# Kernel tuning notes

Measured on AMD Instinct MI355X. Metric: run time of the kernel, lower is better.

The kernel has to match this reference:

```python
import jax, jax.numpy as jnp
import numpy as np

N_NODES = 50000
N_EDGES = 600000
HIDDEN = 128


def setup_inputs() -> dict:
    key = jax.random.key(0)
    ks = jax.random.split(key, 8)
    x = jax.random.normal(ks[0], (N_NODES, HIDDEN), dtype=jnp.float32)
    edge_index = jax.random.randint(ks[1], (2, N_EDGES), 0, N_NODES, dtype=jnp.int32)
    s = 1.0 / np.sqrt(HIDDEN)
    # PyG SAGEConv: lin_l applied to aggregated neighbors (with bias), lin_r to root (no bias)
    W1l = jax.random.uniform(ks[2], (HIDDEN, HIDDEN), jnp.float32, -s, s)
    b1l = jax.random.uniform(ks[3], (HIDDEN,), jnp.float32, -s, s)
    W1r = jax.random.uniform(ks[4], (HIDDEN, HIDDEN), jnp.float32, -s, s)
    W2l = jax.random.uniform(ks[5], (HIDDEN, HIDDEN), jnp.float32, -s, s)
    b2l = jax.random.uniform(ks[6], (HIDDEN,), jnp.float32, -s, s)
    W2r = jax.random.uniform(ks[7], (HIDDEN, HIDDEN), jnp.float32, -s, s)
    return {"x": x, "edge_index": edge_index, "W1l": W1l, "b1l": b1l,
            "W1r": W1r, "W2l": W2l, "b2l": b2l, "W2r": W2r}


def _sage_conv(x, src, dst, Wl, bl, Wr):
    # mean aggregation of source features at destination nodes
    msg_sum = jax.ops.segment_sum(x[src], dst, num_segments=N_NODES)  # [N, H]
    deg = jax.ops.segment_sum(jnp.ones((src.shape[0],), x.dtype), dst,
                              num_segments=N_NODES)  # [N]
    agg = msg_sum / jnp.maximum(deg, 1.0)[:, None]
    return agg @ Wl.T + bl + x @ Wr.T


def reference(x, edge_index, W1l, b1l, W1r, W2l, b2l, W2r):
    src, dst = edge_index[0], edge_index[1]
    h = jax.nn.relu(_sage_conv(x, src, dst, W1l, b1l, W1r))
    out = _sage_conv(h, src, dst, W2l, b2l, W2r)
    return out
```

## Files before the change

kernel.cpp:

```cpp
#include <hip/hip_runtime.h>
#include <hip/hip_bf16.h>

#define N_NODES 50000
#define N_EDGES 600000
#define HID 128
#define SCAN_BLOCKS ((N_NODES + 255) / 256)

typedef __attribute__((ext_vector_type(8))) __bf16 bf16x8;
typedef __attribute__((ext_vector_type(4))) float f32x4;

static __device__ __forceinline__ unsigned short f2b(float v) {
    return __builtin_bit_cast(unsigned short, (__bf16)v);
}


#define NCAST (N_NODES * HID / 8)
#define NVT   (2 * 128 * 256 / 8)
#define NFILL (N_NODES / 4)
#define NPREP (NCAST + NVT + NFILL)

__global__ __launch_bounds__(256) void k_prep(const float* __restrict__ x,
                                              const float* __restrict__ W1l, const float* __restrict__ W1r,
                                              const float* __restrict__ W2l, const float* __restrict__ W2r,
                                              unsigned short* __restrict__ xb,
                                              unsigned short* __restrict__ V1,
                                              unsigned short* __restrict__ V2,
                                              int* __restrict__ fill) {
    int idx = blockIdx.x * 256 + threadIdx.x;
    if (idx < NCAST) {
        const float4* xp = (const float4*)(x + (size_t)idx * 8);
        float4 a = xp[0], b = xp[1];
        uint4 o;
        o.x = f2b(a.x) | ((unsigned)f2b(a.y) << 16);
        o.y = f2b(a.z) | ((unsigned)f2b(a.w) << 16);
        o.z = f2b(b.x) | ((unsigned)f2b(b.y) << 16);
        o.w = f2b(b.z) | ((unsigned)f2b(b.w) << 16);
        *(uint4*)(xb + (size_t)idx * 8) = o;
    } else if (idx < NCAST + NVT) {
        int t = idx - NCAST;
        int i0 = t * 8;
        int which = i0 >> 15;
        const float* Wl = which ? W2l : W1l;
        const float* Wr = which ? W2r : W1r;
        unsigned short* V = which ? V2 : V1;
        int ii = i0 & 32767;
        int j = ii >> 8, k0 = ii & 255;
        const float* Wp = (k0 < HID) ? (Wl + j * HID + k0) : (Wr + j * HID + (k0 - HID));
        const float4* wp4 = (const float4*)Wp;
        float4 a = wp4[0], b = wp4[1];
        uint4 o;
        o.x = f2b(a.x) | ((unsigned)f2b(a.y) << 16);
        o.y = f2b(a.z) | ((unsigned)f2b(a.w) << 16);
        o.z = f2b(b.x) | ((unsigned)f2b(b.y) << 16);
        o.w = f2b(b.z) | ((unsigned)f2b(b.w) << 16);
        *(uint4*)(V + ii) = o;
    } else if (idx < NPREP) {
        int z = idx - (NCAST + NVT);
        *(int4*)(fill + z * 4) = make_int4(0, 0, 0, 0);
    }
}


__global__ void k_deg(const int* __restrict__ dst, int* __restrict__ fill, int ne) {
    int e = blockIdx.x * blockDim.x + threadIdx.x;
    if (e < ne) atomicAdd(&fill[dst[e]], 1);
}

__global__ __launch_bounds__(256) void k_bsum(const int* __restrict__ fill, int* __restrict__ bsum, int n) {
    __shared__ int s[256];
    int tid = threadIdx.x;
    int i = blockIdx.x * 256 + tid;
    s[tid] = (i < n) ? fill[i] : 0;
    __syncthreads();
#pragma unroll
    for (int off = 128; off > 0; off >>= 1) {
        if (tid < off) s[tid] += s[tid + off];
        __syncthreads();
    }
    if (tid == 0) bsum[blockIdx.x] = s[0];
}

__global__ __launch_bounds__(256) void k_scan_bsum(int* __restrict__ bsum, int* __restrict__ row_off,
                                                   int nb, int n) {
    __shared__ int s[256];
    int tid = threadIdx.x;
    int v = (tid < nb) ? bsum[tid] : 0;
    s[tid] = v;
    __syncthreads();
#pragma unroll
    for (int off = 1; off < 256; off <<= 1) {
        int t = (tid >= off) ? s[tid - off] : 0;
        __syncthreads();
        s[tid] += t;
        __syncthreads();
    }
    if (tid < nb) bsum[tid] = s[tid] - v;
    if (tid == 255) row_off[n] = s[255];
}

__global__ __launch_bounds__(256) void k_write_off(int* __restrict__ fill, const int* __restrict__ bsum,
                                                   int* __restrict__ row_off, float* __restrict__ inv_deg,
                                                   int n) {
    __shared__ int s[256];
    int tid = threadIdx.x;
    int i = blockIdx.x * 256 + tid;
    int c = (i < n) ? fill[i] : 0;
    s[tid] = c;
    __syncthreads();
#pragma unroll
    for (int off = 1; off < 256; off <<= 1) {
        int t = (tid >= off) ? s[tid - off] : 0;
        __syncthreads();
        s[tid] += t;
        __syncthreads();
    }
    if (i < n) {
        row_off[i] = bsum[blockIdx.x] + s[tid] - c;
        inv_deg[i] = 1.0f / (float)max(c, 1);
        fill[i] = 0;
    }
}

__global__ void k_place(const int* __restrict__ src, const int* __restrict__ dst,
                        const int* __restrict__ row_off, int* __restrict__ fill,
                        int* __restrict__ csr, int ne) {
    int e = blockIdx.x * blockDim.x + threadIdx.x;
    if (e < ne) {
        int d = dst[e];
        int pos = atomicAdd(&fill[d], 1);
        csr[row_off[d] + pos] = src[e];
    }
}


static __device__ __forceinline__ void acc_bf2(uint2 v, float& a0, float& a1, float& a2, float& a3) {
    a0 += __uint_as_float(v.x << 16);
    a1 += __uint_as_float(v.x & 0xffff0000u);
    a2 += __uint_as_float(v.y << 16);
    a3 += __uint_as_float(v.y & 0xffff0000u);
}

__global__ __launch_bounds__(256) void k_agg(const unsigned short* __restrict__ xb,
                                             const int* __restrict__ csr,
                                             const int* __restrict__ row_off,
                                             const float* __restrict__ inv_deg,
                                             unsigned short* __restrict__ aggB, int n) {
    int g = (blockIdx.x * blockDim.x + threadIdx.x) >> 5;
    int lane = threadIdx.x & 31;
    if (g >= n) return;
    int e0 = row_off[g], e1 = row_off[g + 1];
    float a0 = 0.f, a1 = 0.f, a2 = 0.f, a3 = 0.f;
    int e = e0;
    for (; e + 4 <= e1; e += 4) {
        int s0 = csr[e + 0];
        int s1 = csr[e + 1];
        int s2 = csr[e + 2];
        int s3 = csr[e + 3];
        uint2 v0 = *(const uint2*)(xb + (size_t)s0 * HID + lane * 4);
        uint2 v1 = *(const uint2*)(xb + (size_t)s1 * HID + lane * 4);
        uint2 v2 = *(const uint2*)(xb + (size_t)s2 * HID + lane * 4);
        uint2 v3 = *(const uint2*)(xb + (size_t)s3 * HID + lane * 4);
        acc_bf2(v0, a0, a1, a2, a3);
        acc_bf2(v1, a0, a1, a2, a3);
        acc_bf2(v2, a0, a1, a2, a3);
        acc_bf2(v3, a0, a1, a2, a3);
    }
    if (e + 2 <= e1) {
        int s0 = csr[e + 0];
        int s1 = csr[e + 1];
        uint2 v0 = *(const uint2*)(xb + (size_t)s0 * HID + lane * 4);
        uint2 v1 = *(const uint2*)(xb + (size_t)s1 * HID + lane * 4);
        acc_bf2(v0, a0, a1, a2, a3);
        acc_bf2(v1, a0, a1, a2, a3);
        e += 2;
    }
    if (e < e1) {
        int s0 = csr[e];
        uint2 v0 = *(const uint2*)(xb + (size_t)s0 * HID + lane * 4);
        acc_bf2(v0, a0, a1, a2, a3);
    }
    float inv = inv_deg[g];
    ushort4 o;
    o.x = f2b(a0 * inv); o.y = f2b(a1 * inv); o.z = f2b(a2 * inv); o.w = f2b(a3 * inv);
    *(ushort4*)(aggB + (size_t)g * HID + lane * 4) = o;
}


__global__ __launch_bounds__(512) void k_gemm(const unsigned short* __restrict__ aggB,
                                              const unsigned short* __restrict__ xinB,
                                              const unsigned short* __restrict__ VT,
                                              const float* __restrict__ bias,
                                              float* __restrict__ outF,
                                              unsigned short* __restrict__ outB,
                                              int mode ,
                                              int nrows) {
    __shared__ char As[32768];
    __shared__ char Bs[32768];
    int tid = threadIdx.x;
    int w = tid >> 6, l = tid & 63;
    int r0 = blockIdx.x * 128;

    f32x4 acc[8] = {};

    int arow = w * 16 + (l & 15);
    int kgrp = (l >> 4) * 8;

    for (int p = 0; p < 2; ++p) {
        const unsigned short* Asrc = p ? xinB : aggB;
#pragma unroll
        for (int q = 0; q < 4; ++q) {
            int c = tid + q * 512;
            int m = c >> 4, c16 = c & 15;
            int gr = r0 + m;
            uint4 v = make_uint4(0, 0, 0, 0);
            if (gr < nrows) v = *(const uint4*)(Asrc + (size_t)gr * HID + c16 * 8);
            int byt = (m * 256 + c16 * 16) ^ ((m & 7) << 4);
            *(uint4*)(As + byt) = v;
        }
#pragma unroll
        for (int q = 0; q < 4; ++q) {
            int c = tid + q * 512;
            int j = c >> 4, c16 = c & 15;
            uint4 v = *(const uint4*)(VT + (size_t)j * 256 + p * 128 + c16 * 8);
            int byt = (j * 256 + c16 * 16) ^ ((j & 7) << 4);
            *(uint4*)(Bs + byt) = v;
        }
        __syncthreads();

#pragma unroll
        for (int s = 0; s < 4; ++s) {
            int koff = (s * 32 + kgrp) * 2;
            bf16x8 a = *(const bf16x8*)(As + ((arow * 256 + koff) ^ ((arow & 7) << 4)));
#pragma unroll
            for (int cc = 0; cc < 8; ++cc) {
                int brow = cc * 16 + (l & 15);
                bf16x8 b = *(const bf16x8*)(Bs + ((brow * 256 + koff) ^ ((brow & 7) << 4)));
                acc[cc] = __builtin_amdgcn_mfma_f32_16x16x32_bf16(a, b, acc[cc], 0, 0, 0);
            }
        }
        __syncthreads();
    }

    int lo = l & 15, hi = l >> 4;
#pragma unroll
    for (int cc = 0; cc < 8; ++cc) {
        int col = cc * 16 + lo;
        float bv = bias[col];
#pragma unroll
        for (int i = 0; i < 4; ++i) {
            int gr = r0 + w * 16 + hi * 4 + i;
            if (gr < nrows) {
                float v = acc[cc][i] + bv;
                if (mode) {
                    v = fmaxf(v, 0.f);
                    outB[(size_t)gr * HID + col] = f2b(v);
                } else {
                    outF[(size_t)gr * HID + col] = v;
                }
            }
        }
    }
}


extern "C" void kernel_launch(void* const* d_in, const int* in_sizes, int n_in,
                              void* d_out, int out_size, void* d_ws, size_t ws_size,
                              hipStream_t stream) {
    const float* x   = (const float*)d_in[0];
    const int*   ei  = (const int*)d_in[1];
    const float* W1l = (const float*)d_in[2];
    const float* b1l = (const float*)d_in[3];
    const float* W1r = (const float*)d_in[4];
    const float* W2l = (const float*)d_in[5];
    const float* b2l = (const float*)d_in[6];
    const float* W2r = (const float*)d_in[7];
    float* out = (float*)d_out;

    const int* src = ei;
    const int* dst = ei + N_EDGES;

    char* w = (char*)d_ws;
    unsigned short* aggB = (unsigned short*)(w);
    unsigned short* buf0 = (unsigned short*)(w + 12800000);
    int*   csr     = (int*)(w + 25600000);
    int*   row_off = (int*)(w + 28000000);
    int*   fill    = (int*)(w + 28200192);
    float* inv_deg = (float*)(w + 28400384);
    unsigned short* V1 = (unsigned short*)(w + 28600576);
    unsigned short* V2 = (unsigned short*)(w + 28666112);
    int*   bsum    = (int*)(w + 28731648);

    k_prep<<<(NPREP + 255) / 256, 256, 0, stream>>>(x, W1l, W1r, W2l, W2r, buf0, V1, V2, fill);

    k_deg<<<(N_EDGES + 255) / 256, 256, 0, stream>>>(dst, fill, N_EDGES);

    k_bsum<<<SCAN_BLOCKS, 256, 0, stream>>>(fill, bsum, N_NODES);
    k_scan_bsum<<<1, 256, 0, stream>>>(bsum, row_off, SCAN_BLOCKS, N_NODES);
    k_write_off<<<SCAN_BLOCKS, 256, 0, stream>>>(fill, bsum, row_off, inv_deg, N_NODES);

    k_place<<<(N_EDGES + 255) / 256, 256, 0, stream>>>(src, dst, row_off, fill, csr, N_EDGES);

    const int gemm_grid = (N_NODES + 127) / 128;

    k_agg<<<(N_NODES * 32 + 255) / 256, 256, 0, stream>>>(buf0, csr, row_off, inv_deg, aggB, N_NODES);
    k_gemm<<<gemm_grid, 512, 0, stream>>>(aggB, buf0, V1, b1l, out, buf0, 1, N_NODES);

    k_agg<<<(N_NODES * 32 + 255) / 256, 256, 0, stream>>>(buf0, csr, row_off, inv_deg, aggB, N_NODES);
    k_gemm<<<gemm_grid, 512, 0, stream>>>(aggB, buf0, V2, b2l, out, buf0, 0, N_NODES);
}
```

Before: 157.3 us.

## Merge offset scan into one atomic-cursor kernel, widen gather unroll, prefetch GEMM second half

The three-kernel scan (block sums, scan of sums, write offsets) is replaced by one kernel. Each block reserves its base offset through an atomicAdd on a global cursor, and per-node degree is stored so row ends come from start plus degree. Aggregation now unrolls the gather by 8 with a predicated tail, and the GEMM issues the global loads for the root-feature half into registers before the MFMA loop on the aggregated half runs. These changes cut launch count and expose more memory-level parallelism, at the cost of a non-monotonic CSR block order and higher register pressure.

```diff
diff --git a/kernel.cpp b/kernel.cpp
--- a/kernel.cpp
+++ b/kernel.cpp
@@ -25,7 +25,8 @@
                                               unsigned short* __restrict__ xb,
                                               unsigned short* __restrict__ V1,
                                               unsigned short* __restrict__ V2,
-                                              int* __restrict__ fill) {
+                                              int* __restrict__ fill,
+                                              int* __restrict__ cursor) {
     int idx = blockIdx.x * 256 + threadIdx.x;
     if (idx < NCAST) {
         const float4* xp = (const float4*)(x + (size_t)idx * 8);
@@ -57,6 +58,8 @@
     } else if (idx < NPREP) {
         int z = idx - (NCAST + NVT);
         *(int4*)(fill + z * 4) = make_int4(0, 0, 0, 0);
+    } else if (idx == NPREP) {
+        *cursor = 0;
     }
 }
 
@@ -66,26 +69,17 @@
     if (e < ne) atomicAdd(&fill[dst[e]], 1);
 }
 
-__global__ __launch_bounds__(256) void k_bsum(const int* __restrict__ fill, int* __restrict__ bsum, int n) {
+__global__ __launch_bounds__(256) void k_offsets(int* __restrict__ fill,
+                                                 int* __restrict__ row_start,
+                                                 int* __restrict__ dg,
+                                                 float* __restrict__ inv_deg,
+                                                 int* __restrict__ cursor, int n) {
     __shared__ int s[256];
+    __shared__ int base;
     int tid = threadIdx.x;
     int i = blockIdx.x * 256 + tid;
-    s[tid] = (i < n) ? fill[i] : 0;
-    __syncthreads();
-#pragma unroll
-    for (int off = 128; off > 0; off >>= 1) {
-        if (tid < off) s[tid] += s[tid + off];
-        __syncthreads();
-    }
-    if (tid == 0) bsum[blockIdx.x] = s[0];
-}
-
-__global__ __launch_bounds__(256) void k_scan_bsum(int* __restrict__ bsum, int* __restrict__ row_off,
-                                                   int nb, int n) {
-    __shared__ int s[256];
-    int tid = threadIdx.x;
-    int v = (tid < nb) ? bsum[tid] : 0;
-    s[tid] = v;
+    int c = (i < n) ? fill[i] : 0;
+    s[tid] = c;
     __syncthreads();
 #pragma unroll
     for (int off = 1; off < 256; off <<= 1) {
@@ -94,41 +88,24 @@
         s[tid] += t;
         __syncthreads();
     }
-    if (tid < nb) bsum[tid] = s[tid] - v;
-    if (tid == 255) row_off[n] = s[255];
-}
-
-__global__ __launch_bounds__(256) void k_write_off(int* __restrict__ fill, const int* __restrict__ bsum,
-                                                   int* __restrict__ row_off, float* __restrict__ inv_deg,
-                                                   int n) {
-    __shared__ int s[256];
-    int tid = threadIdx.x;
-    int i = blockIdx.x * 256 + tid;
-    int c = (i < n) ? fill[i] : 0;
-    s[tid] = c;
-    __syncthreads();
-#pragma unroll
-    for (int off = 1; off < 256; off <<= 1) {
-        int t = (tid >= off) ? s[tid - off] : 0;
-        __syncthreads();
-        s[tid] += t;
-        __syncthreads();
-    }
+    if (tid == 255) base = atomicAdd(cursor, s[255]);
+    __syncthreads();
     if (i < n) {
-        row_off[i] = bsum[blockIdx.x] + s[tid] - c;
+        row_start[i] = base + s[tid] - c;
+        dg[i] = c;
         inv_deg[i] = 1.0f / (float)max(c, 1);
         fill[i] = 0;
     }
 }
 
 __global__ void k_place(const int* __restrict__ src, const int* __restrict__ dst,
-                        const int* __restrict__ row_off, int* __restrict__ fill,
+                        const int* __restrict__ row_start, int* __restrict__ fill,
                         int* __restrict__ csr, int ne) {
     int e = blockIdx.x * blockDim.x + threadIdx.x;
     if (e < ne) {
         int d = dst[e];
         int pos = atomicAdd(&fill[d], 1);
-        csr[row_off[d] + pos] = src[e];
+        csr[row_start[d] + pos] = src[e];
     }
 }
 
@@ -142,42 +119,41 @@
 
 __global__ __launch_bounds__(256) void k_agg(const unsigned short* __restrict__ xb,
                                              const int* __restrict__ csr,
-                                             const int* __restrict__ row_off,
+                                             const int* __restrict__ row_start,
+                                             const int* __restrict__ dg,
                                              const float* __restrict__ inv_deg,
                                              unsigned short* __restrict__ aggB, int n) {
     int g = (blockIdx.x * blockDim.x + threadIdx.x) >> 5;
     int lane = threadIdx.x & 31;
     if (g >= n) return;
-    int e0 = row_off[g], e1 = row_off[g + 1];
+    int e0 = row_start[g];
+    int e1 = e0 + dg[g];
     float a0 = 0.f, a1 = 0.f, a2 = 0.f, a3 = 0.f;
     int e = e0;
-    for (; e + 4 <= e1; e += 4) {
-        int s0 = csr[e + 0];
-        int s1 = csr[e + 1];
-        int s2 = csr[e + 2];
-        int s3 = csr[e + 3];
+    for (; e + 8 <= e1; e += 8) {
+        int s0 = csr[e + 0], s1 = csr[e + 1], s2 = csr[e + 2], s3 = csr[e + 3];
+        int s4 = csr[e + 4], s5 = csr[e + 5], s6 = csr[e + 6], s7 = csr[e + 7];
         uint2 v0 = *(const uint2*)(xb + (size_t)s0 * HID + lane * 4);
         uint2 v1 = *(const uint2*)(xb + (size_t)s1 * HID + lane * 4);
         uint2 v2 = *(const uint2*)(xb + (size_t)s2 * HID + lane * 4);
         uint2 v3 = *(const uint2*)(xb + (size_t)s3 * HID + lane * 4);
-        acc_bf2(v0, a0, a1, a2, a3);
-        acc_bf2(v1, a0, a1, a2, a3);
-        acc_bf2(v2, a0, a1, a2, a3);
-        acc_bf2(v3, a0, a1, a2, a3);
-    }
-    if (e + 2 <= e1) {
-        int s0 = csr[e + 0];
-        int s1 = csr[e + 1];
-        uint2 v0 = *(const uint2*)(xb + (size_t)s0 * HID + lane * 4);
-        uint2 v1 = *(const uint2*)(xb + (size_t)s1 * HID + lane * 4);
-        acc_bf2(v0, a0, a1, a2, a3);
-        acc_bf2(v1, a0, a1, a2, a3);
-        e += 2;
+        uint2 v4 = *(const uint2*)(xb + (size_t)s4 * HID + lane * 4);
+        uint2 v5 = *(const uint2*)(xb + (size_t)s5 * HID + lane * 4);
+        uint2 v6 = *(const uint2*)(xb + (size_t)s6 * HID + lane * 4);
+        uint2 v7 = *(const uint2*)(xb + (size_t)s7 * HID + lane * 4);
+        acc_bf2(v0, a0, a1, a2, a3); acc_bf2(v1, a0, a1, a2, a3);
+        acc_bf2(v2, a0, a1, a2, a3); acc_bf2(v3, a0, a1, a2, a3);
+        acc_bf2(v4, a0, a1, a2, a3); acc_bf2(v5, a0, a1, a2, a3);
+        acc_bf2(v6, a0, a1, a2, a3); acc_bf2(v7, a0, a1, a2, a3);
     }
     if (e < e1) {
-        int s0 = csr[e];
-        uint2 v0 = *(const uint2*)(xb + (size_t)s0 * HID + lane * 4);
-        acc_bf2(v0, a0, a1, a2, a3);
+#pragma unroll
+        for (int j = 0; j < 7; ++j) {
+            int ee = e + j;
+            int ss = csr[ee < e1 ? ee : e0];
+            uint2 v = *(const uint2*)(xb + (size_t)ss * HID + lane * 4);
+            if (ee < e1) acc_bf2(v, a0, a1, a2, a3);
+        }
     }
     float inv = inv_deg[g];
     ushort4 o;
@@ -201,44 +177,71 @@
     int r0 = blockIdx.x * 128;
 
     f32x4 acc[8] = {};
-
     int arow = w * 16 + (l & 15);
     int kgrp = (l >> 4) * 8;
 
-    for (int p = 0; p < 2; ++p) {
-        const unsigned short* Asrc = p ? xinB : aggB;
-#pragma unroll
-        for (int q = 0; q < 4; ++q) {
-            int c = tid + q * 512;
-            int m = c >> 4, c16 = c & 15;
-            int gr = r0 + m;
-            uint4 v = make_uint4(0, 0, 0, 0);
-            if (gr < nrows) v = *(const uint4*)(Asrc + (size_t)gr * HID + c16 * 8);
-            int byt = (m * 256 + c16 * 16) ^ ((m & 7) << 4);
-            *(uint4*)(As + byt) = v;
+    int mq[4], cq[4], bytq[4];
+#pragma unroll
+    for (int q = 0; q < 4; ++q) {
+        int c = tid + q * 512;
+        mq[q] = c >> 4;
+        cq[q] = c & 15;
+        bytq[q] = (mq[q] * 256 + cq[q] * 16) ^ ((mq[q] & 7) << 4);
+    }
+
+#pragma unroll
+    for (int q = 0; q < 4; ++q) {
+        int gr = r0 + mq[q];
+        uint4 v = make_uint4(0, 0, 0, 0);
+        if (gr < nrows) v = *(const uint4*)(aggB + (size_t)gr * HID + cq[q] * 8);
+        *(uint4*)(As + bytq[q]) = v;
+    }
+#pragma unroll
+    for (int q = 0; q < 4; ++q) {
+        uint4 v = *(const uint4*)(VT + (size_t)mq[q] * 256 + cq[q] * 8);
+        *(uint4*)(Bs + bytq[q]) = v;
+    }
+    __syncthreads();
+
+    uint4 pa[4], pb[4];
+#pragma unroll
+    for (int q = 0; q < 4; ++q) {
+        int gr = r0 + mq[q];
+        pa[q] = make_uint4(0, 0, 0, 0);
+        if (gr < nrows) pa[q] = *(const uint4*)(xinB + (size_t)gr * HID + cq[q] * 8);
+        pb[q] = *(const uint4*)(VT + (size_t)mq[q] * 256 + 128 + cq[q] * 8);
+    }
+
+#pragma unroll
+    for (int s = 0; s < 4; ++s) {
+        int koff = (s * 32 + kgrp) * 2;
+        bf16x8 a = *(const bf16x8*)(As + ((arow * 256 + koff) ^ ((arow & 7) << 4)));
+#pragma unroll
+        for (int cc = 0; cc < 8; ++cc) {
+            int brow = cc * 16 + (l & 15);
+            bf16x8 b = *(const bf16x8*)(Bs + ((brow * 256 + koff) ^ ((brow & 7) << 4)));
+            acc[cc] = __builtin_amdgcn_mfma_f32_16x16x32_bf16(a, b, acc[cc], 0, 0, 0);
         }
-#pragma unroll
-        for (int q = 0; q < 4; ++q) {
-            int c = tid + q * 512;
-            int j = c >> 4, c16 = c & 15;
-            uint4 v = *(const uint4*)(VT + (size_t)j * 256 + p * 128 + c16 * 8);
-            int byt = (j * 256 + c16 * 16) ^ ((j & 7) << 4);
-            *(uint4*)(Bs + byt) = v;
+    }
+    __syncthreads();
+
+#pragma unroll
+    for (int q = 0; q < 4; ++q) {
+        *(uint4*)(As + bytq[q]) = pa[q];
+        *(uint4*)(Bs + bytq[q]) = pb[q];
+    }
+    __syncthreads();
+
+#pragma unroll
+    for (int s = 0; s < 4; ++s) {
+        int koff = (s * 32 + kgrp) * 2;
+        bf16x8 a = *(const bf16x8*)(As + ((arow * 256 + koff) ^ ((arow & 7) << 4)));
+#pragma unroll
+        for (int cc = 0; cc < 8; ++cc) {
+            int brow = cc * 16 + (l & 15);
+            bf16x8 b = *(const bf16x8*)(Bs + ((brow * 256 + koff) ^ ((brow & 7) << 4)));
+            acc[cc] = __builtin_amdgcn_mfma_f32_16x16x32_bf16(a, b, acc[cc], 0, 0, 0);
         }
-        __syncthreads();
-
-#pragma unroll
-        for (int s = 0; s < 4; ++s) {
-            int koff = (s * 32 + kgrp) * 2;
-            bf16x8 a = *(const bf16x8*)(As + ((arow * 256 + koff) ^ ((arow & 7) << 4)));
-#pragma unroll
-            for (int cc = 0; cc < 8; ++cc) {
-                int brow = cc * 16 + (l & 15);
-                bf16x8 b = *(const bf16x8*)(Bs + ((brow * 256 + koff) ^ ((brow & 7) << 4)));
-                acc[cc] = __builtin_amdgcn_mfma_f32_16x16x32_bf16(a, b, acc[cc], 0, 0, 0);
-            }
-        }
-        __syncthreads();
     }
 
     int lo = l & 15, hi = l >> 4;
@@ -286,25 +289,24 @@
     int*   row_off = (int*)(w + 28000000);
     int*   fill    = (int*)(w + 28200192);
     float* inv_deg = (float*)(w + 28400384);
-    unsigned short* V1 = (unsigned short*)(w + 28600576);
-    unsigned short* V2 = (unsigned short*)(w + 28666112);
-    int*   bsum    = (int*)(w + 28731648);
-
-    k_prep<<<(NPREP + 255) / 256, 256, 0, stream>>>(x, W1l, W1r, W2l, W2r, buf0, V1, V2, fill);
+    int*   dg      = (int*)(w + 28600576);
+    unsigned short* V1 = (unsigned short*)(w + 28800768);
+    unsigned short* V2 = (unsigned short*)(w + 28866304);
+    int*   cursor  = (int*)(w + 28931840);
+
+    k_prep<<<(NPREP + 1 + 255) / 256, 256, 0, stream>>>(x, W1l, W1r, W2l, W2r, buf0, V1, V2, fill, cursor);
 
     k_deg<<<(N_EDGES + 255) / 256, 256, 0, stream>>>(dst, fill, N_EDGES);
 
-    k_bsum<<<SCAN_BLOCKS, 256, 0, stream>>>(fill, bsum, N_NODES);
-    k_scan_bsum<<<1, 256, 0, stream>>>(bsum, row_off, SCAN_BLOCKS, N_NODES);
-    k_write_off<<<SCAN_BLOCKS, 256, 0, stream>>>(fill, bsum, row_off, inv_deg, N_NODES);
+    k_offsets<<<SCAN_BLOCKS, 256, 0, stream>>>(fill, row_off, dg, inv_deg, cursor, N_NODES);
 
     k_place<<<(N_EDGES + 255) / 256, 256, 0, stream>>>(src, dst, row_off, fill, csr, N_EDGES);
 
     const int gemm_grid = (N_NODES + 127) / 128;
 
-    k_agg<<<(N_NODES * 32 + 255) / 256, 256, 0, stream>>>(buf0, csr, row_off, inv_deg, aggB, N_NODES);
+    k_agg<<<(N_NODES * 32 + 255) / 256, 256, 0, stream>>>(buf0, csr, row_off, dg, inv_deg, aggB, N_NODES);
     k_gemm<<<gemm_grid, 512, 0, stream>>>(aggB, buf0, V1, b1l, out, buf0, 1, N_NODES);
 
-    k_agg<<<(N_NODES * 32 + 255) / 256, 256, 0, stream>>>(buf0, csr, row_off, inv_deg, aggB, N_NODES);
+    k_agg<<<(N_NODES * 32 + 255) / 256, 256, 0, stream>>>(buf0, csr, row_off, dg, inv_deg, aggB, N_NODES);
     k_gemm<<<gemm_grid, 512, 0, stream>>>(aggB, buf0, V2, b2l, out, buf0, 0, N_NODES);
 }
```

After: 165.6 us. 5.2% more time.
